# Kernel tuning notes

Hardware: AMD Instinct MI355X
Metric: run time of the kernel (lower is better)

Reference implementation:

```python
import jax, jax.numpy as jnp
import numpy as np

TS = 0.01  # Euler step size (module's `ts`)

N_X, N_U, N_FEAT = 32, 16, 512
BATCH, SEQ_LEN = 512, 2048


def setup_inputs() -> dict:
    key = jax.random.key(0)
    k0, k1, k2, k3 = jax.random.split(key, 4)
    x0_batch = jax.random.normal(k0, (BATCH, 1, N_X), dtype=jnp.float32)
    u_batch = jax.random.normal(k1, (BATCH, SEQ_LEN, N_U), dtype=jnp.float32)
    # 2-layer MLP state-space model: Linear(n_x+n_u, n_feat) -> Tanh -> Linear(n_feat, n_x)
    fan1 = N_X + N_U
    W1 = jax.random.normal(k2, (fan1, N_FEAT), dtype=jnp.float32) / np.sqrt(fan1).astype(np.float32)
    b1 = jnp.zeros((N_FEAT,), dtype=jnp.float32)
    W2 = jax.random.normal(k3, (N_FEAT, N_X), dtype=jnp.float32) / np.sqrt(N_FEAT).astype(np.float32)
    b2 = jnp.zeros((N_X,), dtype=jnp.float32)
    return {"x0_batch": x0_batch, "u_batch": u_batch, "W1": W1, "b1": b1, "W2": W2, "b2": b2}


def reference(x0_batch, u_batch, W1, b1, W2, b2):
    # x0_batch: (B, 1, n_x); u_batch: (B, T, n_u) -> out: (B, T, n_x)
    x0 = x0_batch[:, 0, :]                       # (B, n_x)
    u_t = jnp.swapaxes(u_batch, 0, 1)            # (T, B, n_u) for scan over time

    def step(x, u):
        h = jnp.tanh(jnp.concatenate([x, u], axis=-1) @ W1 + b1)  # (B, n_feat)
        dx = h @ W2 + b2                                           # (B, n_x)
        x_next = x + TS * dx
        return x_next, x_next

    _, xs = jax.lax.scan(step, x0, u_t)          # xs: (T, B, n_x)
    return jnp.swapaxes(xs, 0, 1)                # (B, T, n_x)
```

## Files before the change

### kernel.cpp

```cpp
#include <hip/hip_runtime.h>

typedef float v2f __attribute__((ext_vector_type(2)));

constexpr int NX = 32, NU = 16, NF = 512;
constexpr int SEQ = 2048;
constexpr int NT = 256;
constexpr float SC  = 2.88539008177792681f;
constexpr float TSC = 0.01f;

template<int CTRL>
__device__ __forceinline__ float dpp_mov(float v) {
    return __int_as_float(__builtin_amdgcn_update_dpp(0, __float_as_int(v), CTRL, 0xF, 0xF, true));
}

__device__ __forceinline__ float tanh4(float y) {
    const float e = __builtin_amdgcn_exp2f(y);
    const float r = __builtin_amdgcn_rcpf(e + 1.f);
    return fmaf(-2.f, r, 1.f);
}

__global__ __launch_bounds__(NT)
__attribute__((amdgpu_waves_per_eu(2, 2)))
void fes_kernel(const float* __restrict__ x0, const float* __restrict__ ug,
                const float* __restrict__ W1, const float* __restrict__ b1,
                const float* __restrict__ W2, const float* __restrict__ b2,
                float* __restrict__ out)
{
    __shared__ __align__(16) float xs_w[4][NX];
    __shared__ __align__(16) float part[2][NX][4];

    const int tid = threadIdx.x, row = blockIdx.x;
    const int l = tid & 63, w = tid >> 6;

    const int pi = ((l & 1) << 4) | (((l >> 1) & 1) << 3) | (((l >> 3) & 1) << 2)
                 | (((l >> 4) & 1) << 1) | ((l >> 5) & 1);
    const bool jown = (l & 4) == 0;

    const int f0 = 2 * tid, f1 = f0 + 1;

    v2f wkA[24], wkB[24];
#pragma unroll
    for (int p = 0; p < 24; ++p) {
        wkA[p] = v2f{SC * W1[(2 * p) * NF + f0], SC * W1[(2 * p + 1) * NF + f0]};
        wkB[p] = v2f{SC * W1[(2 * p) * NF + f1], SC * W1[(2 * p + 1) * NF + f1]};
    }
    const float b1A = SC * b1[f0], b1B = SC * b1[f1];

    v2f wcA[16], wcB[16];
#pragma unroll
    for (int m = 0; m < 16; ++m) {
        wcA[m] = v2f{TSC * W2[f0 * NX + ((2 * m) ^ pi)], TSC * W2[f0 * NX + ((2 * m + 1) ^ pi)]};
        wcB[m] = v2f{TSC * W2[f1 * NX + ((2 * m) ^ pi)], TSC * W2[f1 * NX + ((2 * m + 1) ^ pi)]};
    }
    const float bb = TSC * b2[pi];
    float xr = x0[row * NX + pi];

    const float* ug_row  = ug  + (size_t)row * SEQ * NU;
    float*       out_row = out + (size_t)row * SEQ * NX;

    if (jown) xs_w[w][pi] = xr;
    float4 u0 = *(const float4*)(ug_row + 0);
    float4 u1 = *(const float4*)(ug_row + 4);
    float4 u2 = *(const float4*)(ug_row + 8);
    float4 u3 = *(const float4*)(ug_row + 12);

    const float4* xsr = (const float4*)xs_w[w];

#pragma unroll 1
    for (int t = 0; t < SEQ; ++t) {
        v2f aA0 = {b1A, 0.f}, aA1 = {0.f, 0.f};
        v2f aB0 = {b1B, 0.f}, aB1 = {0.f, 0.f};
#pragma unroll
        for (int s = 0; s < 8; ++s) {
            const float4 iv = xsr[s];
            const v2f lo = {iv.x, iv.y}, hi = {iv.z, iv.w};
            aA0 += wkA[2 * s] * lo;  aA1 += wkA[2 * s + 1] * hi;
            aB0 += wkB[2 * s] * lo;  aB1 += wkB[2 * s + 1] * hi;
        }
#define UPART(uv, p0)                                                       \
        { const v2f lo = {uv.x, uv.y}, hi = {uv.z, uv.w};                   \
          aA0 += wkA[p0] * lo;  aA1 += wkA[p0 + 1] * hi;                    \
          aB0 += wkB[p0] * lo;  aB1 += wkB[p0 + 1] * hi; }
        UPART(u0, 16) UPART(u1, 18) UPART(u2, 20) UPART(u3, 22)
#undef UPART
        {
            const int tn = (t + 1 < SEQ) ? t + 1 : SEQ - 1;
            const float* un = ug_row + (size_t)tn * NU;
            u0 = *(const float4*)(un + 0);
            u1 = *(const float4*)(un + 4);
            u2 = *(const float4*)(un + 8);
            u3 = *(const float4*)(un + 12);
        }
        const float h0 = tanh4((aA0.x + aA0.y) + (aA1.x + aA1.y));
        const float h1 = tanh4((aB0.x + aB0.y) + (aB1.x + aB1.y));

        const v2f h0v = {h0, h0}, h1v = {h1, h1};
        v2f q[16];
#pragma unroll
        for (int m = 0; m < 16; ++m)
            q[m] = h0v * wcA[m] + h1v * wcB[m];

#pragma unroll
        for (int m = 0; m < 8; ++m) {
            q[m].x += dpp_mov<0xB1>(q[m + 8].x);
            q[m].y += dpp_mov<0xB1>(q[m + 8].y);
        }
#pragma unroll
        for (int m = 0; m < 4; ++m) {
            q[m].x += dpp_mov<0x4E>(q[m + 4].x);
            q[m].y += dpp_mov<0x4E>(q[m + 4].y);
        }
#pragma unroll
        for (int m = 0; m < 2; ++m) {
            q[m].x += dpp_mov<0x128>(q[m + 2].x);
            q[m].y += dpp_mov<0x128>(q[m + 2].y);
        }
        q[0].x += __shfl_xor(q[1].x, 16);
        q[0].y += __shfl_xor(q[1].y, 16);
        q[0].x += __shfl_xor(q[0].y, 32);
        q[0].x += __shfl_xor(q[0].x, 4);
        const float S = q[0].x;

        if (jown) part[t & 1][pi][w] = S;
        __syncthreads();
        const float4 P = *(const float4*)part[t & 1][pi];
        xr += ((P.x + P.y) + (P.z + P.w)) + bb;

        if (jown) xs_w[w][pi] = xr;
        if (w == 0 && jown) out_row[(size_t)t * NX + pi] = xr;
    }
}

extern "C" void kernel_launch(void* const* d_in, const int* in_sizes, int n_in,
                              void* d_out, int out_size, void* d_ws, size_t ws_size,
                              hipStream_t stream) {
    const float* x0 = (const float*)d_in[0];
    const float* ug = (const float*)d_in[1];
    const float* W1 = (const float*)d_in[2];
    const float* b1 = (const float*)d_in[3];
    const float* W2 = (const float*)d_in[4];
    const float* b2 = (const float*)d_in[5];
    float* out = (float*)d_out;

    fes_kernel<<<dim3(512), dim3(NT), 0, stream>>>(x0, ug, W1, b1, W2, b2, out);
}
```

Baseline: 1.712 ms.

## Broadcast state via cross-lane permutes instead of LDS and use permlane swaps

Each lane now keeps all 32 state values in registers, rebuilt each step from its own updated value through permlane16/32 swaps and DPP moves, so the per-wave LDS round trip for the state vector goes away. The W1 state weights are reordered to match the XOR-permuted register layout. Cross-row shuffle reductions now use permlane swaps instead of ds_bpermute-based shfl. Every lane writes a partial to a padded 8-slot LDS buffer that is read with eight scalar loads, and the input prefetch of u is dropped in favour of loading at the start of each step. In exchange the kernel uses more registers and more cross-lane operations per step.

Result: slower. 2.007 ms (+17.2%).

```diff
diff --git a/kernel.cpp b/kernel.cpp
--- a/kernel.cpp
+++ b/kernel.cpp
@@ -1,6 +1,7 @@
 #include <hip/hip_runtime.h>
 
 typedef float v2f __attribute__((ext_vector_type(2)));
+typedef unsigned uv2 __attribute__((ext_vector_type(2)));
 
 constexpr int NX = 32, NU = 16, NF = 512;
 constexpr int SEQ = 2048;
@@ -11,6 +12,14 @@
 template<int CTRL>
 __device__ __forceinline__ float dpp_mov(float v) {
     return __int_as_float(__builtin_amdgcn_update_dpp(0, __float_as_int(v), CTRL, 0xF, 0xF, true));
+}
+__device__ __forceinline__ float sum16(float v) {
+    uv2 r = __builtin_amdgcn_permlane16_swap(__float_as_uint(v), __float_as_uint(v), false, false);
+    return __uint_as_float(r.x) + __uint_as_float(r.y);
+}
+__device__ __forceinline__ float sum32(float v) {
+    uv2 r = __builtin_amdgcn_permlane32_swap(__float_as_uint(v), __float_as_uint(v), false, false);
+    return __uint_as_float(r.x) + __uint_as_float(r.y);
 }
 
 __device__ __forceinline__ float tanh4(float y) {
@@ -26,23 +35,31 @@
                 const float* __restrict__ W2, const float* __restrict__ b2,
                 float* __restrict__ out)
 {
-    __shared__ __align__(16) float xs_w[4][NX];
-    __shared__ __align__(16) float part[2][NX][4];
+    __shared__ float part[2][8][33];
 
     const int tid = threadIdx.x, row = blockIdx.x;
     const int l = tid & 63, w = tid >> 6;
 
     const int pi = ((l & 1) << 4) | (((l >> 1) & 1) << 3) | (((l >> 3) & 1) << 2)
                  | (((l >> 4) & 1) << 1) | ((l >> 5) & 1);
-    const bool jown = (l & 4) == 0;
+    const int slot = w * 2 + ((l >> 2) & 1);
+    const bool store_lane = (w == 0) && ((l & 4) == 0);
 
     const int f0 = 2 * tid, f1 = f0 + 1;
 
-    v2f wkA[24], wkB[24];
+    v2f wxA[16], wxB[16];
 #pragma unroll
-    for (int p = 0; p < 24; ++p) {
-        wkA[p] = v2f{SC * W1[(2 * p) * NF + f0], SC * W1[(2 * p + 1) * NF + f0]};
-        wkB[p] = v2f{SC * W1[(2 * p) * NF + f1], SC * W1[(2 * p + 1) * NF + f1]};
+    for (int m = 0; m < 16; ++m) {
+        const int ja = pi ^ (2 * m), jb = pi ^ (2 * m + 1);
+        wxA[m] = v2f{SC * W1[ja * NF + f0], SC * W1[jb * NF + f0]};
+        wxB[m] = v2f{SC * W1[ja * NF + f1], SC * W1[jb * NF + f1]};
+    }
+    v2f wuA[8], wuB[8];
+#pragma unroll
+    for (int p = 0; p < 8; ++p) {
+        const int k = NX + 2 * p;
+        wuA[p] = v2f{SC * W1[k * NF + f0], SC * W1[(k + 1) * NF + f0]};
+        wuB[p] = v2f{SC * W1[k * NF + f1], SC * W1[(k + 1) * NF + f1]};
     }
     const float b1A = SC * b1[f0], b1B = SC * b1[f1];
 
@@ -53,44 +70,36 @@
         wcB[m] = v2f{TSC * W2[f1 * NX + ((2 * m) ^ pi)], TSC * W2[f1 * NX + ((2 * m + 1) ^ pi)]};
     }
     const float bb = TSC * b2[pi];
-    float xr = x0[row * NX + pi];
+
+    float xg[32];
+#pragma unroll
+    for (int r = 0; r < 32; ++r) xg[r] = x0[row * NX + (pi ^ r)];
 
     const float* ug_row  = ug  + (size_t)row * SEQ * NU;
     float*       out_row = out + (size_t)row * SEQ * NX;
 
-    if (jown) xs_w[w][pi] = xr;
-    float4 u0 = *(const float4*)(ug_row + 0);
-    float4 u1 = *(const float4*)(ug_row + 4);
-    float4 u2 = *(const float4*)(ug_row + 8);
-    float4 u3 = *(const float4*)(ug_row + 12);
-
-    const float4* xsr = (const float4*)xs_w[w];
-
 #pragma unroll 1
     for (int t = 0; t < SEQ; ++t) {
+        const float* up = ug_row + (size_t)t * NU;
+        const float4 u0 = *(const float4*)(up + 0);
+        const float4 u1 = *(const float4*)(up + 4);
+        const float4 u2 = *(const float4*)(up + 8);
+        const float4 u3 = *(const float4*)(up + 12);
+
         v2f aA0 = {b1A, 0.f}, aA1 = {0.f, 0.f};
         v2f aB0 = {b1B, 0.f}, aB1 = {0.f, 0.f};
 #pragma unroll
-        for (int s = 0; s < 8; ++s) {
-            const float4 iv = xsr[s];
-            const v2f lo = {iv.x, iv.y}, hi = {iv.z, iv.w};
-            aA0 += wkA[2 * s] * lo;  aA1 += wkA[2 * s + 1] * hi;
-            aB0 += wkB[2 * s] * lo;  aB1 += wkB[2 * s + 1] * hi;
+        for (int m = 0; m < 16; ++m) {
+            const v2f xv = {xg[2 * m], xg[2 * m + 1]};
+            if (m & 1) { aA1 += wxA[m] * xv; aB1 += wxB[m] * xv; }
+            else       { aA0 += wxA[m] * xv; aB0 += wxB[m] * xv; }
         }
-#define UPART(uv, p0)                                                       \
+#define UPAIR(uv, p)                                                        \
         { const v2f lo = {uv.x, uv.y}, hi = {uv.z, uv.w};                   \
-          aA0 += wkA[p0] * lo;  aA1 += wkA[p0 + 1] * hi;                    \
-          aB0 += wkB[p0] * lo;  aB1 += wkB[p0 + 1] * hi; }
-        UPART(u0, 16) UPART(u1, 18) UPART(u2, 20) UPART(u3, 22)
-#undef UPART
-        {
-            const int tn = (t + 1 < SEQ) ? t + 1 : SEQ - 1;
-            const float* un = ug_row + (size_t)tn * NU;
-            u0 = *(const float4*)(un + 0);
-            u1 = *(const float4*)(un + 4);
-            u2 = *(const float4*)(un + 8);
-            u3 = *(const float4*)(un + 12);
-        }
+          aA0 += wuA[p] * lo;  aA1 += wuA[p + 1] * hi;                      \
+          aB0 += wuB[p] * lo;  aB1 += wuB[p + 1] * hi; }
+        UPAIR(u0, 0) UPAIR(u1, 2) UPAIR(u2, 4) UPAIR(u3, 6)
+#undef UPAIR
         const float h0 = tanh4((aA0.x + aA0.y) + (aA1.x + aA1.y));
         const float h1 = tanh4((aB0.x + aB0.y) + (aB1.x + aB1.y));
 
@@ -115,19 +124,29 @@
             q[m].x += dpp_mov<0x128>(q[m + 2].x);
             q[m].y += dpp_mov<0x128>(q[m + 2].y);
         }
-        q[0].x += __shfl_xor(q[1].x, 16);
-        q[0].y += __shfl_xor(q[1].y, 16);
-        q[0].x += __shfl_xor(q[0].y, 32);
-        q[0].x += __shfl_xor(q[0].x, 4);
-        const float S = q[0].x;
+        const float S0 = q[0].x + (sum16(q[1].x) - q[1].x);
+        const float S1 = q[0].y + (sum16(q[1].y) - q[1].y);
+        const float S = S0 + (sum32(S1) - S1);
 
-        if (jown) part[t & 1][pi][w] = S;
+        part[t & 1][slot][pi] = S;
         __syncthreads();
-        const float4 P = *(const float4*)part[t & 1][pi];
-        xr += ((P.x + P.y) + (P.z + P.w)) + bb;
+        const float* pb = &part[t & 1][0][pi];
+        const float p0 = pb[0],   p1 = pb[33],  p2 = pb[66],  p3 = pb[99];
+        const float p4 = pb[132], p5 = pb[165], p6 = pb[198], p7 = pb[231];
+        const float dx = (((p0 + p1) + (p2 + p3)) + ((p4 + p5) + (p6 + p7))) + bb;
+        const float xn = xg[0] + dx;
+        if (store_lane) out_row[(size_t)t * NX + pi] = xn;
 
-        if (jown) xs_w[w][pi] = xr;
-        if (w == 0 && jown) out_row[(size_t)t * NX + pi] = xr;
+        xg[0] = xn;
+        xg[1] = sum32(xg[0]) - xg[0];
+        xg[2] = sum16(xg[0]) - xg[0];
+        xg[3] = sum16(xg[1]) - xg[1];
+#pragma unroll
+        for (int r = 0; r < 4; ++r)  xg[4 + r]  = dpp_mov<0x128>(xg[r]);
+#pragma unroll
+        for (int r = 0; r < 8; ++r)  xg[8 + r]  = dpp_mov<0x4E>(xg[r]);
+#pragma unroll
+        for (int r = 0; r < 16; ++r) xg[16 + r] = dpp_mov<0xB1>(xg[r]);
     }
 }
 
```
